# Performance work log

Hardware: AMD Instinct MI355X
Metric: run time of the kernel (lower is better)

Reference implementation:

```python
import jax, jax.numpy as jnp
import numpy as np

D_MODEL, NHEAD, D_K = 512, 8, 64
MIN_RBF, MAX_RBF = 0.1, 0.9
MIN_SPREAD, MAX_SPREAD, BASE = 1.0, 6.0, 20.0
LN_EPS = 1e-5


def _layernorm(x, w, b):
    mu = jnp.mean(x, axis=-1, keepdims=True)
    var = jnp.var(x, axis=-1, keepdims=True)
    return (x - mu) * jax.lax.rsqrt(var + LN_EPS) * w + b


def setup_inputs() -> dict:
    key = jax.random.key(0)
    ks = jax.random.split(key, 10)
    B, N = 1, 2048
    inp = {
        "q": jax.random.normal(ks[0], (B, N, D_MODEL), jnp.float32),
        "k": jax.random.normal(ks[1], (B, N, D_MODEL), jnp.float32),
        "v": jax.random.normal(ks[2], (B, N, D_MODEL), jnp.float32),
        "coords": jax.random.normal(ks[3], (B, N, 3), jnp.float32) * 3.0,
        "key_padding_mask": jnp.zeros((B, N), bool),
        # learned params (torch.randn init for projections, LN defaults)
        "q_proj": jax.random.normal(ks[4], (NHEAD, D_MODEL, D_K), jnp.float32),
        "k_proj": jax.random.normal(ks[5], (NHEAD, D_MODEL, D_K), jnp.float32),
        "v_proj": jax.random.normal(ks[6], (NHEAD, D_MODEL, D_K), jnp.float32),
        "q_ln_w": jnp.ones((D_K,), jnp.float32), "q_ln_b": jnp.zeros((D_K,), jnp.float32),
        "k_ln_w": jnp.ones((D_K,), jnp.float32), "k_ln_b": jnp.zeros((D_K,), jnp.float32),
        "v_ln_w": jnp.ones((D_K,), jnp.float32), "v_ln_b": jnp.zeros((D_K,), jnp.float32),
        "out_w": jax.random.normal(ks[7], (D_MODEL, D_MODEL), jnp.float32) / np.sqrt(D_MODEL),
        "out_b": jnp.zeros((D_MODEL,), jnp.float32),
    }
    return inp


def reference(q, k, v, coords, key_padding_mask,
              q_proj, k_proj, v_proj,
              q_ln_w, q_ln_b, k_ln_w, k_ln_b, v_ln_w, v_ln_b,
              out_w, out_b):
    B, N, _ = q.shape
    # per-head projections: [B,H,N,dk]
    Q = _layernorm(jnp.einsum('bnd,hdk->bhnk', q, q_proj), q_ln_w, q_ln_b)
    K = _layernorm(jnp.einsum('bnd,hdk->bhnk', k, k_proj), k_ln_w, k_ln_b)
    V = _layernorm(jnp.einsum('bnd,hdk->bhnk', v, v_proj), v_ln_w, v_ln_b)

    # head-specific gaussian spreads (torch.logspace(0,1,H,base) semantics)
    spreads = MIN_SPREAD + (MAX_SPREAD - MIN_SPREAD) * (BASE ** jnp.linspace(0.0, 1.0, NHEAD) - 1.0) / (BASE - 1.0)

    # pairwise squared distances [B,N,N] -> per-head RBF [B,H,N,N]
    d2 = jnp.sum((coords[:, :, None, :] - coords[:, None, :, :]) ** 2, axis=-1)
    rbf = jnp.exp(-d2[:, None, :, :] / (2.0 * spreads[None, :, None, None] ** 2))
    rbf = jnp.clip(rbf, MIN_RBF, MAX_RBF)

    # RBF-modulated scaled dot-product attention
    scores = jnp.einsum('bhik,bhjk->bhij', Q, K) / np.sqrt(D_K) * rbf
    scores = jnp.where(key_padding_mask[:, None, None, :], -1e9, scores)
    P = jax.nn.softmax(scores, axis=-1)
    out = jnp.einsum('bhij,bhjk->bhik', P, V)  # [B,H,N,dk]

    # torch: out.permute(0,2,3,1).reshape(B,N,d_model)
    out = jnp.transpose(out, (0, 2, 3, 1)).reshape(B, N, D_MODEL)
    return out @ out_w.T + out_b
```

## Files before the change

kernel.cpp:

```cpp
#include <hip/hip_runtime.h>
#include <math.h>

#define N_TOK 2048
#define D_MODEL 512
#define NHEAD 8
#define DK 64
#define LOG2E 1.44269504f
#define QSCALE 0.18033688f

typedef __attribute__((ext_vector_type(8))) short short8;
typedef __attribute__((ext_vector_type(4))) short short4v;
typedef __attribute__((ext_vector_type(4))) float f32x4;

__device__ __forceinline__ short f2bf(float x) {
    unsigned u = __float_as_uint(x);
    u = (u + 0x7fffu + ((u >> 16) & 1u)) >> 16;
    return (short)u;
}

__device__ __forceinline__ float bf2f(short s) {
    return __uint_as_float(((unsigned)(unsigned short)s) << 16);
}

__device__ __forceinline__ unsigned cvt_pk_bf16(float lo, float hi) {
    unsigned r;
    asm("v_cvt_pk_bf16_f32 %0, %1, %2" : "=v"(r) : "v"(lo), "v"(hi));
    return r;
}

__device__ __forceinline__ float head_c(int h) {
    float tt = (float)h * (1.0f / 7.0f);
    float sp = 1.0f + 5.0f * (__builtin_exp2f(tt * 4.3219281f) - 1.0f) * (1.0f / 19.0f);
    return -LOG2E / (2.0f * sp * sp);
}

__global__ __launch_bounds__(256) void convert_x_kernel(
    const float* __restrict__ q, const float* __restrict__ k,
    const float* __restrict__ v, short* __restrict__ Xbf)
{
    int i = blockIdx.x * 256 + threadIdx.x;
    int t = i >> 17;
    int rem = i & 131071;
    const float4* src = (const float4*)(t == 0 ? q : (t == 1 ? k : v));
    float4 a = src[rem * 2], b = src[rem * 2 + 1];
    short8 o;
    o[0] = f2bf(a.x); o[1] = f2bf(a.y); o[2] = f2bf(a.z); o[3] = f2bf(a.w);
    o[4] = f2bf(b.x); o[5] = f2bf(b.y); o[6] = f2bf(b.z); o[7] = f2bf(b.w);
    *(short8*)(Xbf + (size_t)i * 8) = o;
}

__global__ __launch_bounds__(256) void prep_w_kernel(
    const float* __restrict__ qp, const float* __restrict__ kp,
    const float* __restrict__ vp, const float* __restrict__ ow,
    short* __restrict__ Wt, short* __restrict__ Wo)
{
    const int z = blockIdx.z, t = threadIdx.x;
    if (z == 3) {
        int m0 = blockIdx.x * 64, j0 = blockIdx.y * 64;
        int hh = j0 >> 6;
        for (int i = t; i < 4096; i += 256) {
            int r = i >> 6, kk = i & 63;
            Wo[(size_t)(m0 + r) * 512 + j0 + kk] =
                f2bf(ow[(size_t)(m0 + r) * 512 + kk * 8 + hh]);
        }
        return;
    }
    const float* src = z == 0 ? qp : (z == 1 ? kp : vp);
    __shared__ float tile[64][65];
    const int h = blockIdx.x;
    const int d0 = blockIdx.y * 64;
    for (int i = t; i < 4096; i += 256) {
        int r = i >> 6, c = i & 63;
        tile[r][c] = src[((size_t)h * 512 + d0 + r) * 64 + c];
    }
    __syncthreads();
    short* W = Wt + (size_t)z * 512 * 512;
    for (int i = t; i < 4096; i += 256) {
        int cr = i >> 6, dc_ = i & 63;
        W[(size_t)(h * 64 + cr) * 512 + d0 + dc_] = f2bf(tile[dc_][cr]);
    }
}

__global__ __launch_bounds__(256) void prep_rbf_kernel(
    const float* __restrict__ coords, const unsigned char* __restrict__ mask,
    float4* __restrict__ ck4, float* __restrict__ mpen, unsigned* __restrict__ tflag)
{
    int j = blockIdx.x * 256 + threadIdx.x;
    float x = coords[j * 3 + 0], y = coords[j * 3 + 1], z = coords[j * 3 + 2];
    unsigned char mk = mask[j];
    mpen[j] = mk ? -1e9f : 0.f;
    unsigned long long b = __ballot(mk != 0);
    if ((threadIdx.x & 63) == 0) tflag[j >> 6] = (b != 0ull) ? 1u : 0u;
    float n2 = x * x + y * y + z * z;
    #pragma unroll
    for (int h = 0; h < NHEAD; ++h) {
        float c = head_c(h);
        float4 o; o.x = -2.f * c * x; o.y = -2.f * c * y; o.z = -2.f * c * z; o.w = c * n2;
        ck4[(size_t)h * N_TOK + j] = o;
    }
}

__global__ __launch_bounds__(256) void proj_ln_mfma_kernel(
    const short* __restrict__ Xbf, const short* __restrict__ Wt,
    const float* __restrict__ qlw, const float* __restrict__ qlb,
    const float* __restrict__ klw, const float* __restrict__ klb,
    const float* __restrict__ vlw, const float* __restrict__ vlb,
    short* __restrict__ Qbf, short* __restrict__ Kf, short* __restrict__ Vf)
{
    __shared__ short Xs[64 * 64];
    __shared__ short Ws[64 * 64];
    const int z = blockIdx.z, h = blockIdx.y;
    const int n0 = blockIdx.x * 64;
    const int tid = threadIdx.x, w = tid >> 6, l = tid & 63;
    const int l15 = l & 15, lg = l >> 4;

    const short* X = Xbf + (size_t)z * N_TOK * D_MODEL;
    const short* Wz = Wt + ((size_t)z * 512 + h * 64) * 512;

    const f32x4 zero4 = {0.f, 0.f, 0.f, 0.f};
    f32x4 acc[4];
    #pragma unroll
    for (int dc = 0; dc < 4; ++dc) acc[dc] = zero4;

    for (int kb = 0; kb < 8; ++kb) {
        const int d0 = kb * 64;
        __syncthreads();
        #pragma unroll
        for (int i = 0; i < 2; ++i) {
            int c = tid + i * 256;
            int r = c >> 3, g = c & 7;
            short8 xv = *(const short8*)(X + (size_t)(n0 + r) * 512 + d0 + g * 8);
            *(short8*)(Xs + r * 64 + ((g * 8) ^ ((r & 7) << 3))) = xv;
            short8 wv = *(const short8*)(Wz + (size_t)r * 512 + d0 + g * 8);
            *(short8*)(Ws + r * 64 + ((g * 8) ^ ((r & 7) << 3))) = wv;
        }
        __syncthreads();
        const int arow = w * 16 + l15;
        short8 a0 = *(const short8*)(Xs + arow * 64 + ((lg * 8) ^ ((arow & 7) << 3)));
        short8 a1 = *(const short8*)(Xs + arow * 64 + ((32 + lg * 8) ^ ((arow & 7) << 3)));
        #pragma unroll
        for (int dc = 0; dc < 4; ++dc) {
            const int brow = dc * 16 + l15;
            short8 b0 = *(const short8*)(Ws + brow * 64 + ((lg * 8) ^ ((brow & 7) << 3)));
            acc[dc] = __builtin_amdgcn_mfma_f32_16x16x32_bf16(a0, b0, acc[dc], 0, 0, 0);
            short8 b1 = *(const short8*)(Ws + brow * 64 + ((32 + lg * 8) ^ ((brow & 7) << 3)));
            acc[dc] = __builtin_amdgcn_mfma_f32_16x16x32_bf16(a1, b1, acc[dc], 0, 0, 0);
        }
    }

    const float* lw  = z == 0 ? qlw : (z == 1 ? klw : vlw);
    const float* lbp = z == 0 ? qlb : (z == 1 ? klb : vlb);
    float wv_[4], bv_[4];
    #pragma unroll
    for (int dc = 0; dc < 4; ++dc) {
        wv_[dc] = lw[dc * 16 + l15];
        bv_[dc] = lbp[dc * 16 + l15];
    }
    float mu[4], rs[4];
    #pragma unroll
    for (int reg = 0; reg < 4; ++reg) {
        float s = acc[0][reg] + acc[1][reg] + acc[2][reg] + acc[3][reg];
        #pragma unroll
        for (int off = 1; off < 16; off <<= 1) s += __shfl_xor(s, off);
        float m = s * (1.0f / 64.0f);
        float ss = 0.f;
        #pragma unroll
        for (int dc = 0; dc < 4; ++dc) { float d = acc[dc][reg] - m; ss += d * d; }
        #pragma unroll
        for (int off = 1; off < 16; off <<= 1) ss += __shfl_xor(ss, off);
        mu[reg] = m;
        rs[reg] = rsqrtf(ss * (1.0f / 64.0f) + 1e-5f);
    }

    const int tile = n0 >> 6;
    if (z == 0) {
        #pragma unroll
        for (int dc = 0; dc < 4; ++dc)
            #pragma unroll
            for (int reg = 0; reg < 4; ++reg) {
                int n = n0 + w * 16 + lg * 4 + reg;
                float val = ((acc[dc][reg] - mu[reg]) * rs[reg] * wv_[dc] + bv_[dc]) * QSCALE;
                Qbf[((size_t)h * N_TOK + n) * DK + dc * 16 + l15] = f2bf(val);
            }
    } else if (z == 1) {
        short* Kh = Kf + (size_t)h * N_TOK * DK;
        #pragma unroll
        for (int dc = 0; dc < 4; ++dc) {
            int hf  = dc >> 1;
            int lgc = ((dc & 1) << 1) | (l15 >> 3);
            int e   = l15 & 7;
            size_t base = (size_t)tile * 4096 + (w * 2 + hf) * 512 + 16 * 8 * lgc + e;
            #pragma unroll
            for (int reg = 0; reg < 4; ++reg) {
                float val = (acc[dc][reg] - mu[reg]) * rs[reg] * wv_[dc] + bv_[dc];
                Kh[base + (lg * 4 + reg) * 8] = f2bf(val);
            }
        }
    } else {
        short* Vh = Vf + (size_t)h * N_TOK * DK;
        int hfv = w >> 1;
        int lgv = ((w & 1) << 1) | (lg >> 1);
        int eb  = (lg & 1) * 4;
        #pragma unroll
        for (int dc = 0; dc < 4; ++dc) {
            short4v p;
            #pragma unroll
            for (int reg = 0; reg < 4; ++reg)
                p[reg] = f2bf((acc[dc][reg] - mu[reg]) * rs[reg] * wv_[dc] + bv_[dc]);
            size_t addr = (size_t)tile * 4096 + (dc * 2 + hfv) * 512 + (l15 + 16 * lgv) * 8 + eb;
            *(short4v*)(Vh + addr) = p;
        }
    }
}

__global__ __launch_bounds__(256) void attn_kernel(
    const short* __restrict__ Qbf, const short* __restrict__ Kf,
    const short* __restrict__ Vf, const float* __restrict__ coords,
    const float4* __restrict__ ck4, const float* __restrict__ mpen,
    const unsigned* __restrict__ tflag,
    short* __restrict__ PO, float* __restrict__ PL)
{
    __shared__ short Pls[4][1024];
    __shared__ float bufO[2][64][17];
    __shared__ float bufL[2][64];

    const int tid = threadIdx.x;
    const int w = tid >> 6, l = tid & 63;
    const int l15 = l & 15, lg = l >> 4;
    const int bid = blockIdx.x;
    const int h  = bid & 7;
    const int nt = (bid >> 3) & 127;
    const int z  = bid >> 10;
    const int n0 = nt * 16;

    char* Pb = (char*)&Pls[w][0];
    const int psw = (l15 & 7) << 4;

    const short* Qrow = Qbf + ((size_t)h * N_TOK + n0 + l15) * DK + lg * 8;
    const short8 qf0 = *(const short8*)(Qrow);
    const short8 qf1 = *(const short8*)(Qrow + 32);

    const float ch = head_c(h);
    const float qx = coords[(n0 + l15) * 3 + 0];
    const float qy = coords[(n0 + l15) * 3 + 1];
    const float qz = coords[(n0 + l15) * 3 + 2];
    const float cq2 = ch * (qx * qx + qy * qy + qz * qz);
    const float4* ckh = ck4 + (size_t)h * N_TOK;

    const f32x4 zero4 = {0.f, 0.f, 0.f, 0.f};
    float l_ = 0.f;
    f32x4 oacc[4];
    #pragma unroll
    for (int i = 0; i < 4; ++i) oacc[i] = zero4;

    const short* Kfh = Kf + (size_t)h * N_TOK * DK;
    const short* Vfh = Vf + (size_t)h * N_TOK * DK;

    for (int t = 0; t < 4; ++t) {
        const int kt = (z * 4 + w) * 4 + t;
        const int kbase = kt * 64;
        const short* kp = Kfh + (size_t)kt * 4096 + l * 8;
        const short* vp = Vfh + (size_t)kt * 4096 + l * 8;

        f32x4 sacc[4];
        #pragma unroll
        for (int nc = 0; nc < 4; ++nc) {
            short8 k0 = *(const short8*)(kp + nc * 1024);
            short8 k1 = *(const short8*)(kp + nc * 1024 + 512);
            sacc[nc] = __builtin_amdgcn_mfma_f32_16x16x32_bf16(k0, qf0, zero4, 0, 0, 0);
            sacc[nc] = __builtin_amdgcn_mfma_f32_16x16x32_bf16(k1, qf1, sacc[nc], 0, 0, 0);
        }

        #pragma unroll
        for (int nc = 0; nc < 4; ++nc) {
            #pragma unroll
            for (int reg = 0; reg < 4; ++reg) {
                float4 c4 = ckh[kbase + nc * 16 + lg * 4 + reg];
                float arg = fmaf(c4.x, qx, fmaf(c4.y, qy, fmaf(c4.z, qz, c4.w))) + cq2;
                float rb = __builtin_exp2f(arg);
                rb = fminf(fmaxf(rb, 0.1f), 0.9f);
                sacc[nc][reg] *= rb;
            }
        }
        if (tflag[kt]) {
            #pragma unroll
            for (int nc = 0; nc < 4; ++nc)
                #pragma unroll
                for (int reg = 0; reg < 4; ++reg)
                    sacc[nc][reg] += mpen[kbase + nc * 16 + lg * 4 + reg];
        }

        float ps = 0.f;
        #pragma unroll
        for (int nc = 0; nc < 4; ++nc) {
            float p0 = __builtin_exp2f(sacc[nc][0]);
            float p1 = __builtin_exp2f(sacc[nc][1]);
            float p2 = __builtin_exp2f(sacc[nc][2]);
            float p3 = __builtin_exp2f(sacc[nc][3]);
            ps += (p0 + p1) + (p2 + p3);
            uint2 u;
            u.x = cvt_pk_bf16(p0, p1);
            u.y = cvt_pk_bf16(p2, p3);
            *(uint2*)(Pb + ((l15 * 128 + nc * 32 + lg * 8) ^ psw)) = u;
        }
        ps += __shfl_xor(ps, 16);
        ps += __shfl_xor(ps, 32);
        l_ += ps;

        short8 pf0 = *(const short8*)(Pb + ((l15 * 128 + lg * 16) ^ psw));
        short8 pf1 = *(const short8*)(Pb + ((l15 * 128 + 64 + lg * 16) ^ psw));
        #pragma unroll
        for (int dcc = 0; dcc < 4; ++dcc) {
            short8 v0 = *(const short8*)(vp + dcc * 1024);
            short8 v1 = *(const short8*)(vp + dcc * 1024 + 512);
            oacc[dcc] = __builtin_amdgcn_mfma_f32_16x16x32_bf16(v0, pf0, oacc[dcc], 0, 0, 0);
            oacc[dcc] = __builtin_amdgcn_mfma_f32_16x16x32_bf16(v1, pf1, oacc[dcc], 0, 0, 0);
        }
    }

    if (w >= 2) {
        int slot = w - 2;
        bufL[slot][l] = l_;
        #pragma unroll
        for (int dc = 0; dc < 4; ++dc)
            #pragma unroll
            for (int reg = 0; reg < 4; ++reg)
                bufO[slot][l][dc * 4 + reg] = oacc[dc][reg];
    }
    __syncthreads();
    if (w < 2) {
        l_ += bufL[w][l];
        #pragma unroll
        for (int dc = 0; dc < 4; ++dc)
            #pragma unroll
            for (int reg = 0; reg < 4; ++reg)
                oacc[dc][reg] += bufO[w][l][dc * 4 + reg];
    }
    __syncthreads();
    if (w == 1) {
        bufL[0][l] = l_;
        #pragma unroll
        for (int dc = 0; dc < 4; ++dc)
            #pragma unroll
            for (int reg = 0; reg < 4; ++reg)
                bufO[0][l][dc * 4 + reg] = oacc[dc][reg];
    }
    __syncthreads();
    if (w == 0) {
        float lf = l_ + bufL[0][l];
        size_t p = ((size_t)z * NHEAD + h) * N_TOK + n0 + l15;
        if (lg == 0) PL[p] = lf;
        #pragma unroll
        for (int dcc = 0; dcc < 4; ++dcc) {
            short4v o4;
            #pragma unroll
            for (int reg = 0; reg < 4; ++reg)
                o4[reg] = f2bf(oacc[dcc][reg] + bufO[0][l][dcc * 4 + reg]);
            *(short4v*)(PO + p * 64 + dcc * 16 + lg * 4) = o4;
        }
    }
}

__global__ __launch_bounds__(256) void merge_kernel(
    const short* __restrict__ PO, const float* __restrict__ PL,
    short* __restrict__ ATT)
{
    const int t = threadIdx.x;
    const int u = t >> 6, d = t & 63;
    const int q = blockIdx.x * 4 + u;
    const int h = blockIdx.y;
    const size_t p0 = (size_t)h * N_TOK + q;
    const size_t p1 = (size_t)(NHEAD + h) * N_TOK + q;
    float rl = 1.0f / (PL[p0] + PL[p1]);
    float o0 = bf2f(PO[p0 * 64 + d]), o1 = bf2f(PO[p1 * 64 + d]);
    ATT[(size_t)q * D_MODEL + h * 64 + d] = f2bf((o0 + o1) * rl);
}

__global__ __launch_bounds__(256) void out_proj_kernel(
    const short* __restrict__ ATT, const short* __restrict__ Wo,
    const float* __restrict__ bias, float* __restrict__ out)
{
    __shared__ short As[64 * 64];
    __shared__ short Bs[64 * 64];
    const int n0 = blockIdx.x * 64, m0 = blockIdx.y * 64;
    const int tid = threadIdx.x, w = tid >> 6, l = tid & 63;
    const int l15 = l & 15, lg = l >> 4;

    const f32x4 zero4 = {0.f, 0.f, 0.f, 0.f};
    f32x4 acc[4];
    #pragma unroll
    for (int dc = 0; dc < 4; ++dc) acc[dc] = zero4;

    for (int kb = 0; kb < 8; ++kb) {
        const int j0 = kb * 64;
        __syncthreads();
        #pragma unroll
        for (int i = 0; i < 2; ++i) {
            int c = tid + i * 256;
            int r = c >> 3, g = c & 7;
            short8 av = *(const short8*)(ATT + (size_t)(n0 + r) * 512 + j0 + g * 8);
            *(short8*)(As + r * 64 + ((g * 8) ^ ((r & 7) << 3))) = av;
            short8 bv = *(const short8*)(Wo + (size_t)(m0 + r) * 512 + j0 + g * 8);
            *(short8*)(Bs + r * 64 + ((g * 8) ^ ((r & 7) << 3))) = bv;
        }
        __syncthreads();
        const int arow = w * 16 + l15;
        short8 a0 = *(const short8*)(As + arow * 64 + ((lg * 8) ^ ((arow & 7) << 3)));
        short8 a1 = *(const short8*)(As + arow * 64 + ((32 + lg * 8) ^ ((arow & 7) << 3)));
        #pragma unroll
        for (int dc = 0; dc < 4; ++dc) {
            const int brow = dc * 16 + l15;
            short8 b0 = *(const short8*)(Bs + brow * 64 + ((lg * 8) ^ ((brow & 7) << 3)));
            acc[dc] = __builtin_amdgcn_mfma_f32_16x16x32_bf16(a0, b0, acc[dc], 0, 0, 0);
            short8 b1 = *(const short8*)(Bs + brow * 64 + ((32 + lg * 8) ^ ((brow & 7) << 3)));
            acc[dc] = __builtin_amdgcn_mfma_f32_16x16x32_bf16(a1, b1, acc[dc], 0, 0, 0);
        }
    }

    #pragma unroll
    for (int dc = 0; dc < 4; ++dc) {
        float bm = bias[m0 + dc * 16 + l15];
        #pragma unroll
        for (int reg = 0; reg < 4; ++reg) {
            int n = n0 + w * 16 + lg * 4 + reg;
            out[(size_t)n * D_MODEL + m0 + dc * 16 + l15] = acc[dc][reg] + bm;
        }
    }
}

extern "C" void kernel_launch(void* const* d_in, const int* in_sizes, int n_in,
                              void* d_out, int out_size, void* d_ws, size_t ws_size,
                              hipStream_t stream)
{
    const float* q      = (const float*)d_in[0];
    const float* k      = (const float*)d_in[1];
    const float* v      = (const float*)d_in[2];
    const float* coords = (const float*)d_in[3];
    const unsigned char* mask = (const unsigned char*)d_in[4];
    const float* q_proj = (const float*)d_in[5];
    const float* k_proj = (const float*)d_in[6];
    const float* v_proj = (const float*)d_in[7];
    const float* q_ln_w = (const float*)d_in[8];
    const float* q_ln_b = (const float*)d_in[9];
    const float* k_ln_w = (const float*)d_in[10];
    const float* k_ln_b = (const float*)d_in[11];
    const float* v_ln_w = (const float*)d_in[12];
    const float* v_ln_b = (const float*)d_in[13];
    const float* out_w  = (const float*)d_in[14];
    const float* out_b  = (const float*)d_in[15];
    float* out = (float*)d_out;

    short* Xbf = (short*)d_ws;
    short* Wt  = Xbf + 3145728;
    short* Wo  = Wt + 786432;
    short* Qbf = Wo + 262144;
    short* Kf  = Qbf + 1048576;
    short* Vf  = Kf + 1048576;
    short* ATT = Vf + 1048576;
    float*  fr   = (float*)(ATT + 1048576);
    float4* ck4  = (float4*)fr;
    float*  mpen = fr + 65536;
    unsigned* tflag = (unsigned*)(mpen + 2048);

    short* PO = Xbf;
    float* PL = (float*)Wt;

    convert_x_kernel<<<dim3(1536), dim3(256), 0, stream>>>(q, k, v, Xbf);
    prep_w_kernel<<<dim3(8, 8, 4), dim3(256), 0, stream>>>(q_proj, k_proj, v_proj, out_w, Wt, Wo);
    prep_rbf_kernel<<<dim3(8), dim3(256), 0, stream>>>(coords, mask, ck4, mpen, tflag);
    proj_ln_mfma_kernel<<<dim3(32, 8, 3), dim3(256), 0, stream>>>(
        Xbf, Wt, q_ln_w, q_ln_b, k_ln_w, k_ln_b, v_ln_w, v_ln_b, Qbf, Kf, Vf);
    attn_kernel<<<dim3(2048), dim3(256), 0, stream>>>(
        Qbf, Kf, Vf, coords, ck4, mpen, tflag, PO, PL);
    merge_kernel<<<dim3(512, 8), dim3(256), 0, stream>>>(PO, PL, ATT);
    out_proj_kernel<<<dim3(32, 8), dim3(256), 0, stream>>>(ATT, Wo, out_b, out);
}
```

Measured before the change: 74.32 us.

## Merge prep kernels, fold merge into out-proj, compute row sums via MFMA

Combines the three preprocessing kernels into one launch and removes the separate merge kernel by doing the split-K softmax normalization inside the out-projection A-tile load. The ATT intermediate buffer goes away. The attention row-sum is now computed with an extra MFMA against a ones vector instead of scalar adds and cross-lane shuffles. This trades launch overhead and a global round trip for redundant merge work in the out-projection blocks (each of the 8 column blocks recomputes it) and bf16-rounded row sums.

New measurement: 74.60 us. About the same (+0.4%).

```diff
diff --git a/kernel.cpp b/kernel.cpp
--- a/kernel.cpp
+++ b/kernel.cpp
@@ -34,69 +34,69 @@
     return -LOG2E / (2.0f * sp * sp);
 }
 
-__global__ __launch_bounds__(256) void convert_x_kernel(
+__global__ __launch_bounds__(256) void prep_all_kernel(
     const float* __restrict__ q, const float* __restrict__ k,
-    const float* __restrict__ v, short* __restrict__ Xbf)
-{
-    int i = blockIdx.x * 256 + threadIdx.x;
-    int t = i >> 17;
-    int rem = i & 131071;
-    const float4* src = (const float4*)(t == 0 ? q : (t == 1 ? k : v));
-    float4 a = src[rem * 2], b = src[rem * 2 + 1];
-    short8 o;
-    o[0] = f2bf(a.x); o[1] = f2bf(a.y); o[2] = f2bf(a.z); o[3] = f2bf(a.w);
-    o[4] = f2bf(b.x); o[5] = f2bf(b.y); o[6] = f2bf(b.z); o[7] = f2bf(b.w);
-    *(short8*)(Xbf + (size_t)i * 8) = o;
-}
-
-__global__ __launch_bounds__(256) void prep_w_kernel(
+    const float* __restrict__ v, const float* __restrict__ coords,
+    const unsigned char* __restrict__ mask,
     const float* __restrict__ qp, const float* __restrict__ kp,
     const float* __restrict__ vp, const float* __restrict__ ow,
-    short* __restrict__ Wt, short* __restrict__ Wo)
+    short* __restrict__ Xbf, short* __restrict__ Wt, short* __restrict__ Wo,
+    float4* __restrict__ ck4, float* __restrict__ mpen,
+    unsigned* __restrict__ tflag)
 {
-    const int z = blockIdx.z, t = threadIdx.x;
-    if (z == 3) {
-        int m0 = blockIdx.x * 64, j0 = blockIdx.y * 64;
-        int hh = j0 >> 6;
-        for (int i = t; i < 4096; i += 256) {
-            int r = i >> 6, kk = i & 63;
-            Wo[(size_t)(m0 + r) * 512 + j0 + kk] =
-                f2bf(ow[(size_t)(m0 + r) * 512 + kk * 8 + hh]);
-        }
-        return;
-    }
-    const float* src = z == 0 ? qp : (z == 1 ? kp : vp);
     __shared__ float tile[64][65];
-    const int h = blockIdx.x;
-    const int d0 = blockIdx.y * 64;
-    for (int i = t; i < 4096; i += 256) {
-        int r = i >> 6, c = i & 63;
-        tile[r][c] = src[((size_t)h * 512 + d0 + r) * 64 + c];
-    }
-    __syncthreads();
-    short* W = Wt + (size_t)z * 512 * 512;
-    for (int i = t; i < 4096; i += 256) {
-        int cr = i >> 6, dc_ = i & 63;
-        W[(size_t)(h * 64 + cr) * 512 + d0 + dc_] = f2bf(tile[dc_][cr]);
-    }
-}
-
-__global__ __launch_bounds__(256) void prep_rbf_kernel(
-    const float* __restrict__ coords, const unsigned char* __restrict__ mask,
-    float4* __restrict__ ck4, float* __restrict__ mpen, unsigned* __restrict__ tflag)
-{
-    int j = blockIdx.x * 256 + threadIdx.x;
-    float x = coords[j * 3 + 0], y = coords[j * 3 + 1], z = coords[j * 3 + 2];
-    unsigned char mk = mask[j];
-    mpen[j] = mk ? -1e9f : 0.f;
-    unsigned long long b = __ballot(mk != 0);
-    if ((threadIdx.x & 63) == 0) tflag[j >> 6] = (b != 0ull) ? 1u : 0u;
-    float n2 = x * x + y * y + z * z;
-    #pragma unroll
-    for (int h = 0; h < NHEAD; ++h) {
-        float c = head_c(h);
-        float4 o; o.x = -2.f * c * x; o.y = -2.f * c * y; o.z = -2.f * c * z; o.w = c * n2;
-        ck4[(size_t)h * N_TOK + j] = o;
+    const int bid = blockIdx.x;
+    const int t = threadIdx.x;
+
+    if (bid < 1536) {
+        int i = bid * 256 + t;
+        int tt = i >> 17;
+        int rem = i & 131071;
+        const float4* src = (const float4*)(tt == 0 ? q : (tt == 1 ? k : v));
+        float4 a = src[rem * 2], b = src[rem * 2 + 1];
+        short8 o;
+        o[0] = f2bf(a.x); o[1] = f2bf(a.y); o[2] = f2bf(a.z); o[3] = f2bf(a.w);
+        o[4] = f2bf(b.x); o[5] = f2bf(b.y); o[6] = f2bf(b.z); o[7] = f2bf(b.w);
+        *(short8*)(Xbf + (size_t)i * 8) = o;
+    } else if (bid < 1792) {
+        int i = bid - 1536;
+        int z = i >> 6;
+        int bx = i & 7, by = (i >> 3) & 7;
+        if (z == 3) {
+            int m0 = bx * 64, j0 = by * 64, hh = by;
+            for (int ii = t; ii < 4096; ii += 256) {
+                int r = ii >> 6, kk = ii & 63;
+                Wo[(size_t)(m0 + r) * 512 + j0 + kk] =
+                    f2bf(ow[(size_t)(m0 + r) * 512 + kk * 8 + hh]);
+            }
+            return;
+        }
+        const float* src = z == 0 ? qp : (z == 1 ? kp : vp);
+        const int h = bx, d0 = by * 64;
+        for (int ii = t; ii < 4096; ii += 256) {
+            int r = ii >> 6, c = ii & 63;
+            tile[r][c] = src[((size_t)h * 512 + d0 + r) * 64 + c];
+        }
+        __syncthreads();
+        short* W = Wt + (size_t)z * 512 * 512;
+        for (int ii = t; ii < 4096; ii += 256) {
+            int cr = ii >> 6, dc_ = ii & 63;
+            W[(size_t)(h * 64 + cr) * 512 + d0 + dc_] = f2bf(tile[dc_][cr]);
+        }
+    } else {
+        int j = (bid - 1792) * 256 + t;
+        float x = coords[j * 3 + 0], y = coords[j * 3 + 1], z = coords[j * 3 + 2];
+        unsigned char mk = mask[j];
+        mpen[j] = mk ? -1e9f : 0.f;
+        unsigned long long b = __ballot(mk != 0);
+        if ((t & 63) == 0) tflag[j >> 6] = (b != 0ull) ? 1u : 0u;
+        float n2 = x * x + y * y + z * z;
+        #pragma unroll
+        for (int h = 0; h < NHEAD; ++h) {
+            float c = head_c(h);
+            float4 o; o.x = -2.f * c * x; o.y = -2.f * c * y; o.z = -2.f * c * z; o.w = c * n2;
+            ck4[(size_t)h * N_TOK + j] = o;
+        }
     }
 }
 
@@ -247,9 +247,13 @@
     const float cq2 = ch * (qx * qx + qy * qy + qz * qz);
     const float4* ckh = ck4 + (size_t)h * N_TOK;
 
+    short8 ones8;
+    #pragma unroll
+    for (int i = 0; i < 8; ++i) ones8[i] = (short)0x3F80;
+
     const f32x4 zero4 = {0.f, 0.f, 0.f, 0.f};
-    float l_ = 0.f;
     f32x4 oacc[4];
+    f32x4 oacc_l = zero4;
     #pragma unroll
     for (int i = 0; i < 4; ++i) oacc[i] = zero4;
 
@@ -290,22 +294,17 @@
                     sacc[nc][reg] += mpen[kbase + nc * 16 + lg * 4 + reg];
         }
 
-        float ps = 0.f;
         #pragma unroll
         for (int nc = 0; nc < 4; ++nc) {
             float p0 = __builtin_exp2f(sacc[nc][0]);
             float p1 = __builtin_exp2f(sacc[nc][1]);
             float p2 = __builtin_exp2f(sacc[nc][2]);
             float p3 = __builtin_exp2f(sacc[nc][3]);
-            ps += (p0 + p1) + (p2 + p3);
             uint2 u;
             u.x = cvt_pk_bf16(p0, p1);
             u.y = cvt_pk_bf16(p2, p3);
             *(uint2*)(Pb + ((l15 * 128 + nc * 32 + lg * 8) ^ psw)) = u;
         }
-        ps += __shfl_xor(ps, 16);
-        ps += __shfl_xor(ps, 32);
-        l_ += ps;
 
         short8 pf0 = *(const short8*)(Pb + ((l15 * 128 + lg * 16) ^ psw));
         short8 pf1 = *(const short8*)(Pb + ((l15 * 128 + 64 + lg * 16) ^ psw));
@@ -316,7 +315,11 @@
             oacc[dcc] = __builtin_amdgcn_mfma_f32_16x16x32_bf16(v0, pf0, oacc[dcc], 0, 0, 0);
             oacc[dcc] = __builtin_amdgcn_mfma_f32_16x16x32_bf16(v1, pf1, oacc[dcc], 0, 0, 0);
         }
-    }
+        oacc_l = __builtin_amdgcn_mfma_f32_16x16x32_bf16(ones8, pf0, oacc_l, 0, 0, 0);
+        oacc_l = __builtin_amdgcn_mfma_f32_16x16x32_bf16(ones8, pf1, oacc_l, 0, 0, 0);
+    }
+
+    float l_ = oacc_l[0];
 
     if (w >= 2) {
         int slot = w - 2;
@@ -361,24 +364,10 @@
     }
 }
 
-__global__ __launch_bounds__(256) void merge_kernel(
+__global__ __launch_bounds__(256) void out_proj_kernel(
     const short* __restrict__ PO, const float* __restrict__ PL,
-    short* __restrict__ ATT)
-{
-    const int t = threadIdx.x;
-    const int u = t >> 6, d = t & 63;
-    const int q = blockIdx.x * 4 + u;
-    const int h = blockIdx.y;
-    const size_t p0 = (size_t)h * N_TOK + q;
-    const size_t p1 = (size_t)(NHEAD + h) * N_TOK + q;
-    float rl = 1.0f / (PL[p0] + PL[p1]);
-    float o0 = bf2f(PO[p0 * 64 + d]), o1 = bf2f(PO[p1 * 64 + d]);
-    ATT[(size_t)q * D_MODEL + h * 64 + d] = f2bf((o0 + o1) * rl);
-}
-
-__global__ __launch_bounds__(256) void out_proj_kernel(
-    const short* __restrict__ ATT, const short* __restrict__ Wo,
-    const float* __restrict__ bias, float* __restrict__ out)
+    const short* __restrict__ Wo, const float* __restrict__ bias,
+    float* __restrict__ out)
 {
     __shared__ short As[64 * 64];
     __shared__ short Bs[64 * 64];
@@ -398,7 +387,16 @@
         for (int i = 0; i < 2; ++i) {
             int c = tid + i * 256;
             int r = c >> 3, g = c & 7;
-            short8 av = *(const short8*)(ATT + (size_t)(n0 + r) * 512 + j0 + g * 8);
+            int n = n0 + r;
+            size_t p0 = (size_t)kb * N_TOK + n;
+            size_t p1 = (size_t)(NHEAD + kb) * N_TOK + n;
+            float rl = 1.0f / (PL[p0] + PL[p1]);
+            short8 a0 = *(const short8*)(PO + p0 * 64 + g * 8);
+            short8 a1 = *(const short8*)(PO + p1 * 64 + g * 8);
+            short8 av;
+            #pragma unroll
+            for (int e = 0; e < 8; ++e)
+                av[e] = f2bf((bf2f(a0[e]) + bf2f(a1[e])) * rl);
             *(short8*)(As + r * 64 + ((g * 8) ^ ((r & 7) << 3))) = av;
             short8 bv = *(const short8*)(Wo + (size_t)(m0 + r) * 512 + j0 + g * 8);
             *(short8*)(Bs + r * 64 + ((g * 8) ^ ((r & 7) << 3))) = bv;
@@ -456,8 +454,7 @@
     short* Qbf = Wo + 262144;
     short* Kf  = Qbf + 1048576;
     short* Vf  = Kf + 1048576;
-    short* ATT = Vf + 1048576;
-    float*  fr   = (float*)(ATT + 1048576);
+    float*  fr   = (float*)(Vf + 1048576);
     float4* ck4  = (float4*)fr;
     float*  mpen = fr + 65536;
     unsigned* tflag = (unsigned*)(mpen + 2048);
@@ -465,13 +462,12 @@
     short* PO = Xbf;
     float* PL = (float*)Wt;
 
-    convert_x_kernel<<<dim3(1536), dim3(256), 0, stream>>>(q, k, v, Xbf);
-    prep_w_kernel<<<dim3(8, 8, 4), dim3(256), 0, stream>>>(q_proj, k_proj, v_proj, out_w, Wt, Wo);
-    prep_rbf_kernel<<<dim3(8), dim3(256), 0, stream>>>(coords, mask, ck4, mpen, tflag);
+    prep_all_kernel<<<dim3(1800), dim3(256), 0, stream>>>(
+        q, k, v, coords, mask, q_proj, k_proj, v_proj, out_w,
+        Xbf, Wt, Wo, ck4, mpen, tflag);
     proj_ln_mfma_kernel<<<dim3(32, 8, 3), dim3(256), 0, stream>>>(
         Xbf, Wt, q_ln_w, q_ln_b, k_ln_w, k_ln_b, v_ln_w, v_ln_b, Qbf, Kf, Vf);
     attn_kernel<<<dim3(2048), dim3(256), 0, stream>>>(
         Qbf, Kf, Vf, coords, ck4, mpen, tflag, PO, PL);
-    merge_kernel<<<dim3(512, 8), dim3(256), 0, stream>>>(PO, PL, ATT);
-    out_proj_kernel<<<dim3(32, 8), dim3(256), 0, stream>>>(ATT, Wo, out_b, out);
-}
+    out_proj_kernel<<<dim3(32, 8), dim3(256), 0, stream>>>(PO, PL, Wo, out_b, out);
+}
```
